# Performance work log

Hardware: AMD Instinct MI355X
Metric: run time of the kernel (lower is better)

The kernel has to match this reference:

```python
import jax, jax.numpy as jnp
import numpy as np

B, L, F, D = 128, 64, 3072, 1024
CV, CN = 512, 1024  # verb/noun concept channels
MAX_K = (L + 7) // 8
BN_EPS = 1e-5


def setup_inputs() -> dict:
    key = jax.random.key(0)
    ks = jax.random.split(key, 24)
    s_in = 1.0 / np.sqrt(F)
    s_d = 1.0 / np.sqrt(D)
    inp = {
        'inputs': jax.random.normal(ks[0], (B, L, F), jnp.float32),
        'input_lens': jax.random.randint(ks[1], (B,), 1, L + 1, jnp.int32),
        # three level linear embeds
        'W0': jax.random.normal(ks[2], (F, D), jnp.float32) * s_in,
        'b0': jnp.zeros((D,), jnp.float32),
        'W1': jax.random.normal(ks[3], (F, D), jnp.float32) * s_in,
        'b1': jnp.zeros((D,), jnp.float32),
        'W2': jax.random.normal(ks[4], (F, D), jnp.float32) * s_in,
        'b2': jnp.zeros((D,), jnp.float32),
        # attention scorer
        'w_attn': jax.random.normal(ks[5], (D, 1), jnp.float32) * s_d,
        'b_attn': jnp.zeros((1,), jnp.float32),
        # verb classifier: Conv1d(D, CV, 3, pad=1) + BN + sigmoid
        'Kv': jax.random.normal(ks[6], (CV, D, 3), jnp.float32) * (1.0 / np.sqrt(D * 3)),
        'bv': jnp.zeros((CV,), jnp.float32),
        'g_v': jnp.ones((CV,), jnp.float32),
        'beta_v': jnp.zeros((CV,), jnp.float32),
        'mean_v': jax.random.normal(ks[7], (CV,), jnp.float32) * 0.1,
        'var_v': jax.random.uniform(ks[8], (CV,), jnp.float32, 0.5, 1.5),
        # noun classifier: Conv1d(D, CN, 1) + BN + sigmoid
        'Kn': jax.random.normal(ks[9], (CN, D, 1), jnp.float32) * s_d,
        'bn_b': jnp.zeros((CN,), jnp.float32),
        'g_n': jnp.ones((CN,), jnp.float32),
        'beta_n': jnp.zeros((CN,), jnp.float32),
        'mean_n': jax.random.normal(ks[10], (CN,), jnp.float32) * 0.1,
        'var_n': jax.random.uniform(ks[11], (CN,), jnp.float32, 0.5, 1.5),
    }
    return inp


def _conv_bn_sigmoid(x_bld, K, b, gamma, beta, mean, var, pad):
    # x_bld: (B, L, D) -> permute to NCH (B, D, L) as in torch
    x = jnp.transpose(x_bld, (0, 2, 1))
    y = jax.lax.conv_general_dilated(
        x, K, window_strides=(1,), padding=[(pad, pad)],
        dimension_numbers=('NCH', 'OIH', 'NCH'))
    y = y + b[None, :, None]
    # BatchNorm1d in eval mode (running stats)
    y = (y - mean[None, :, None]) * jax.lax.rsqrt(var + BN_EPS)[None, :, None]
    y = y * gamma[None, :, None] + beta[None, :, None]
    y = jax.nn.sigmoid(y)
    return jnp.transpose(y, (0, 2, 1))  # (B, L, C)


def _topk_mean(logits, input_lens):
    # logits: (B, L, C); per-sample top-ceil(len/8) over time, then mean
    lens = input_lens.astype(jnp.int32)
    kk = (lens + 7) // 8  # (B,)
    valid = (jnp.arange(L)[None, :] < lens[:, None])  # (B, L)
    masked = jnp.where(valid[:, :, None], logits, -1e18)
    # top MAX_K per (batch, class) over time
    top = jax.lax.top_k(jnp.transpose(masked, (0, 2, 1)), MAX_K)[0]  # (B, C, MAX_K)
    take = (jnp.arange(MAX_K)[None, None, :] < kk[:, None, None]).astype(logits.dtype)
    return jnp.sum(top * take, axis=-1) / kk[:, None].astype(logits.dtype)  # (B, C)


def reference(inputs, input_lens, W0, b0, W1, b1, W2, b2, w_attn, b_attn,
              Kv, bv, g_v, beta_v, mean_v, var_v,
              Kn, bn_b, g_n, beta_n, mean_n, var_n):
    # level embeds (dropout is identity in eval)
    e0 = inputs @ W0 + b0
    e1 = inputs @ W1 + b1
    e2 = inputs @ W2 + b2

    # masked softmax attention pooling over time -> sent_embeds
    scores = (e0 @ w_attn)[:, :, 0] + b_attn[0]  # (B, L)
    valid = jnp.arange(L)[None, :] < input_lens[:, None]
    scores = jnp.where(valid, scores, -1e18)
    attn = jax.nn.softmax(scores, axis=1)
    sent_embeds = jnp.sum(e0 * attn[:, :, None], axis=1)  # (B, D)

    logits_verb = _conv_bn_sigmoid(e1, Kv, bv, g_v, beta_v, mean_v, var_v, pad=1)  # (B, L, CV)
    logits_noun = _conv_bn_sigmoid(e2, Kn, bn_b, g_n, beta_n, mean_n, var_n, pad=0)  # (B, L, CN)

    instance_logits_verb = _topk_mean(logits_verb, input_lens)  # (B, CV)
    instance_logits_noun = _topk_mean(logits_noun, input_lens)  # (B, CN)

    return (sent_embeds, e1, e2, instance_logits_verb, instance_logits_noun)
```

## Files before the change

### kernel.cpp

```cpp
#include <hip/hip_runtime.h>
#include <cstdint>
#include <cstddef>

typedef unsigned short u16;
typedef __attribute__((ext_vector_type(8))) short short8;
typedef __attribute__((ext_vector_type(4))) float f32x4;

static __device__ __forceinline__ float bf2f(u16 h) {
  union { unsigned u; float f; } a; a.u = ((unsigned)h) << 16; return a.f;
}
static __device__ __forceinline__ u16 f2bf(float x) {
  union { float f; unsigned u; } a; a.f = x;
  return (u16)((a.u + 0x7fffu + ((a.u >> 16) & 1u)) >> 16);
}

#define GLDS16(gp, lp)                                                          \
  __builtin_amdgcn_global_load_lds(                                             \
      (const __attribute__((address_space(1))) void*)(gp),                      \
      (__attribute__((address_space(3))) void*)(lp), 16, 0, 0)

__global__ void prep_all(const float* __restrict__ inputs, u16* __restrict__ Xbf,
                         const float* __restrict__ W0, const float* __restrict__ W1,
                         const float* __restrict__ W2, u16* __restrict__ Wt,
                         const float* __restrict__ Kv, const float* __restrict__ bv,
                         const float* __restrict__ g_v, const float* __restrict__ beta_v,
                         const float* __restrict__ mean_v, const float* __restrict__ var_v,
                         u16* __restrict__ KVt, float* __restrict__ biasv,
                         const float* __restrict__ Kn, const float* __restrict__ bnb,
                         const float* __restrict__ g_n, const float* __restrict__ beta_n,
                         const float* __restrict__ mean_n, const float* __restrict__ var_n,
                         u16* __restrict__ KNt, float* __restrict__ biasn,
                         u16* __restrict__ e1pad) {
  __shared__ float tile[32][33];
  const int id = blockIdx.x;
  const int tid = threadIdx.x;
  if (id < 24576) {
    const int i = id * 256 + tid;
    float4 v = ((const float4*)inputs)[i];
    ushort4 o;
    o.x = f2bf(v.x); o.y = f2bf(v.y); o.z = f2bf(v.z); o.w = f2bf(v.w);
    ((ushort4*)Xbf)[i] = o;
  } else if (id < 33792) {
    const int idd = id - 24576;
    const int kb = (idd % 96) * 32;
    const int jb = (idd / 96) * 32;
    const int tx = tid & 31, ty = tid >> 5;
    const int w = jb >> 10;
    const float* W = (w == 0) ? W0 : ((w == 1) ? W1 : W2);
    const int nb = jb & 1023;
    for (int i = ty; i < 32; i += 8)
      tile[i][tx] = W[(size_t)(kb + i) * 1024 + nb + tx];
    __syncthreads();
    for (int i = ty; i < 32; i += 8)
      Wt[(size_t)(jb + i) * 3072 + kb + tx] = f2bf(tile[tx][i]);
  } else if (id < 34304) {
    const int c = id - 33792;
    const float scale = g_v[c] * rsqrtf(var_v[c] + 1e-5f);
    for (int t = 0; t < 3; t++)
      for (int d = tid; d < 1024; d += 256)
        KVt[(size_t)c * 3072 + t * 1024 + d] = f2bf(Kv[(size_t)c * 3072 + d * 3 + t] * scale);
    if (tid == 0) biasv[c] = (bv[c] - mean_v[c]) * scale + beta_v[c];
  } else if (id < 35328) {
    const int c = id - 34304;
    const float scale = g_n[c] * rsqrtf(var_n[c] + 1e-5f);
    for (int d = tid; d < 1024; d += 256)
      KNt[(size_t)c * 1024 + d] = f2bf(Kn[(size_t)c * 1024 + d] * scale);
    if (tid == 0) biasn[c] = (bnb[c] - mean_n[c]) * scale + beta_n[c];
  } else {
    const int i = (id - 35328) * 256 + tid;
    const int b = i >> 11;
    const int j = i & 2047;
    const int r = (j < 1024) ? 0 : 65;
    const int d = j & 1023;
    e1pad[(size_t)(b * 66 + r) * 1024 + d] = 0;
  }
}

__global__ void gemm_embed(const u16* __restrict__ A, const u16* __restrict__ Bmat,
                           const float* __restrict__ bias0, const float* __restrict__ bias1,
                           const float* __restrict__ bias2,
                           float* __restrict__ oute1, float* __restrict__ oute2,
                           u16* __restrict__ e0bf, u16* __restrict__ e1pad,
                           u16* __restrict__ e2bf) {
  constexpr int K = 3072;
  __shared__ __align__(16) u16 As[128 * 32];
  __shared__ __align__(16) u16 Bs[128 * 32];

  const int tid = threadIdx.x;
  const int m0 = blockIdx.y * 128;
  const int n0 = blockIdx.x * 128;

  const int srow = tid >> 2;
  const int qlog = ((tid & 3) - (srow >> 1)) & 3;
  const int sq = qlog * 8;

  const u16* aR0 = A + (size_t)(m0 + srow) * 3072;
  const u16* aR1 = A + (size_t)(m0 + 64 + srow) * 3072;
  const u16* bR0 = Bmat + (size_t)(n0 + srow) * 3072;
  const u16* bR1 = Bmat + (size_t)(n0 + 64 + srow) * 3072;

  u16* ldsA0 = &As[tid * 8];
  u16* ldsA1 = &As[tid * 8 + 2048];
  u16* ldsB0 = &Bs[tid * 8];
  u16* ldsB1 = &Bs[tid * 8 + 2048];

  const int lane = tid & 63;
  const int warp = tid >> 6;
  const int wm = warp & 1, wn = warp >> 1;
  const int l15 = lane & 15, quad = lane >> 4;
  const int swz = (quad + (l15 >> 1)) & 3;

  const u16* aF = &As[(wm * 64 + l15) * 32 + swz * 8];
  const u16* bF = &Bs[(wn * 64 + l15) * 32 + swz * 8];

  f32x4 acc[4][4];
#pragma unroll
  for (int i = 0; i < 4; i++)
#pragma unroll
    for (int j = 0; j < 4; j++) acc[i][j] = (f32x4){0.f, 0.f, 0.f, 0.f};

  for (int k0 = 0; k0 < K; k0 += 32) {
    __syncthreads();
    GLDS16(aR0 + k0 + sq, ldsA0);
    GLDS16(aR1 + k0 + sq, ldsA1);
    GLDS16(bR0 + k0 + sq, ldsB0);
    GLDS16(bR1 + k0 + sq, ldsB1);
    __syncthreads();

    short8 fa[4], fb[4];
#pragma unroll
    for (int i = 0; i < 4; i++) fa[i] = *(const short8*)(aF + i * 512);
#pragma unroll
    for (int j = 0; j < 4; j++) fb[j] = *(const short8*)(bF + j * 512);
#pragma unroll
    for (int i = 0; i < 4; i++)
#pragma unroll
      for (int j = 0; j < 4; j++)
        acc[i][j] = __builtin_amdgcn_mfma_f32_16x16x32_bf16(fa[i], fb[j], acc[i][j], 0, 0, 0);
  }

  const int w = n0 >> 10;
  const float* bp = (w == 0) ? bias0 : ((w == 1) ? bias1 : bias2);
#pragma unroll
  for (int i = 0; i < 4; i++) {
    const int mrow = m0 + wm * 64 + i * 16 + quad * 4;
#pragma unroll
    for (int j = 0; j < 4; j++) {
      const int c = n0 + wn * 64 + j * 16 + l15;
      const int n = c & 1023;
      const float bias = bp[n];
#pragma unroll
      for (int r = 0; r < 4; r++) {
        const int m = mrow + r;
        const float v = acc[i][j][r] + bias;
        if (w == 0) {
          e0bf[(size_t)m * 1024 + n] = f2bf(v);
        } else if (w == 1) {
          oute1[(size_t)m * 1024 + n] = v;
          const int bb = m >> 6, ll = m & 63;
          e1pad[(size_t)(bb * 66 + ll + 1) * 1024 + n] = f2bf(v);
        } else {
          oute2[(size_t)m * 1024 + n] = v;
          e2bf[(size_t)m * 1024 + n] = f2bf(v);
        }
      }
    }
  }
}

template<int MODE>
__device__ __forceinline__ void conv_gemm_body(
    int bx, int by, const u16* __restrict__ A, const u16* __restrict__ Bmat,
    const float* __restrict__ bias, const int* __restrict__ lens,
    float* __restrict__ out, u16* As, u16* Bs) {
  constexpr int K = (MODE == 1) ? 3072 : 1024;
  constexpr int ldB = (MODE == 1) ? 3072 : 1024;
  constexpr int NC = (MODE == 1) ? 512 : 1024;

  const int tid = threadIdx.x;
  const int m0 = by * 128;
  const int n0 = bx * 128;

  const int srow = tid >> 2;
  const int qlog = ((tid & 3) - (srow >> 1)) & 3;
  const int sq = qlog * 8;

  const u16* aR0;
  const u16* aR1;
  int rb0 = 0, rb1 = 0;
  if constexpr (MODE == 1) {
    const int bb = m0 >> 6;
    rb0 = (bb * 66 + srow) * 1024;
    rb1 = ((bb + 1) * 66 + srow) * 1024;
    aR0 = A; aR1 = A;
  } else {
    aR0 = A + (size_t)(m0 + srow) * 1024;
    aR1 = A + (size_t)(m0 + 64 + srow) * 1024;
  }
  const u16* bR0 = Bmat + (size_t)(n0 + srow) * ldB;
  const u16* bR1 = Bmat + (size_t)(n0 + 64 + srow) * ldB;

  u16* ldsA0 = &As[tid * 8];
  u16* ldsA1 = &As[tid * 8 + 2048];
  u16* ldsB0 = &Bs[tid * 8];
  u16* ldsB1 = &Bs[tid * 8 + 2048];

  const int lane = tid & 63;
  const int warp = tid >> 6;
  const int wm = warp & 1, wn = warp >> 1;
  const int l15 = lane & 15, quad = lane >> 4;
  const int swz = (quad + (l15 >> 1)) & 3;

  const u16* aF = &As[(wm * 64 + l15) * 32 + swz * 8];
  const u16* bF = &Bs[(wn * 64 + l15) * 32 + swz * 8];

  f32x4 acc[4][4];
#pragma unroll
  for (int i = 0; i < 4; i++)
#pragma unroll
    for (int j = 0; j < 4; j++) acc[i][j] = (f32x4){0.f, 0.f, 0.f, 0.f};

  for (int k0 = 0; k0 < K; k0 += 32) {
    __syncthreads();
    const u16 *ga0, *ga1;
    if constexpr (MODE == 1) {
      const int t = k0 >> 10;
      const int kk = (k0 & 1023) + sq;
      ga0 = A + rb0 + t * 1024 + kk;
      ga1 = A + rb1 + t * 1024 + kk;
    } else {
      ga0 = aR0 + k0 + sq;
      ga1 = aR1 + k0 + sq;
    }
    GLDS16(ga0, ldsA0);
    GLDS16(ga1, ldsA1);
    GLDS16(bR0 + k0 + sq, ldsB0);
    GLDS16(bR1 + k0 + sq, ldsB1);
    __syncthreads();

    short8 fa[4], fb[4];
#pragma unroll
    for (int i = 0; i < 4; i++) fa[i] = *(const short8*)(aF + i * 512);
#pragma unroll
    for (int j = 0; j < 4; j++) fb[j] = *(const short8*)(bF + j * 512);
#pragma unroll
    for (int i = 0; i < 4; i++)
#pragma unroll
      for (int j = 0; j < 4; j++)
        acc[i][j] = __builtin_amdgcn_mfma_f32_16x16x32_bf16(fa[i], fb[j], acc[i][j], 0, 0, 0);
  }

  const int b = (m0 >> 6) + wm;
  const int len = lens[b];
  const int kk8 = (len + 7) >> 3;
#pragma unroll
  for (int j = 0; j < 4; j++) {
    const int c = n0 + wn * 64 + j * 16 + l15;
    const float bias_c = bias[c];
    float t[8];
#pragma unroll
    for (int q8 = 0; q8 < 8; q8++) t[q8] = -1e30f;
#pragma unroll
    for (int i = 0; i < 4; i++) {
#pragma unroll
      for (int r = 0; r < 4; r++) {
        const int l = i * 16 + quad * 4 + r;
        const float v = acc[i][j][r] + bias_c;
        const float sg = 1.0f / (1.0f + __expf(-v));
        float x = (l < len) ? sg : -1e30f;
#pragma unroll
        for (int q8 = 0; q8 < 8; q8++) {
          const float hi = fmaxf(t[q8], x);
          x = fminf(t[q8], x);
          t[q8] = hi;
        }
      }
    }
#pragma unroll
    for (int mask = 16; mask <= 32; mask <<= 1) {
      float xs[8];
#pragma unroll
      for (int q8 = 0; q8 < 8; q8++) xs[q8] = __shfl_xor(t[q8], mask);
#pragma unroll
      for (int q8 = 0; q8 < 8; q8++) {
        float x = xs[q8];
#pragma unroll
        for (int p8 = 0; p8 < 8; p8++) {
          const float hi = fmaxf(t[p8], x);
          x = fminf(t[p8], x);
          t[p8] = hi;
        }
      }
    }
    if (quad == 0) {
      float s = 0.f;
#pragma unroll
      for (int q8 = 0; q8 < 8; q8++) s += (q8 < kk8) ? t[q8] : 0.f;
      out[(size_t)b * NC + c] = s / (float)kk8;
    }
  }
}

__global__ void fused_tail(const u16* __restrict__ e1pad, const u16* __restrict__ KVt,
                           const float* __restrict__ biasv,
                           const u16* __restrict__ e2bf, const u16* __restrict__ KNt,
                           const float* __restrict__ biasn,
                           const u16* __restrict__ e0bf, const float* __restrict__ w_attn,
                           const float* __restrict__ b_attn, const int* __restrict__ lens,
                           float* __restrict__ out_sent, float* __restrict__ out_ilv,
                           float* __restrict__ out_iln) {
  __shared__ __align__(16) u16 smem[2 * 128 * 32 + 256];
  u16* As = smem;
  u16* Bs = smem + 128 * 32;
  const int id = blockIdx.x;
  if (id < 256) {
    conv_gemm_body<1>(id & 3, id >> 2, e1pad, KVt, biasv, lens, out_ilv, As, Bs);
  } else if (id < 768) {
    const int id2 = id - 256;
    conv_gemm_body<2>(id2 & 7, id2 >> 3, e2bf, KNt, biasn, lens, out_iln, As, Bs);
  } else {
    const int b = id - 768;
    const int tid = threadIdx.x;
    const int lane = tid & 63;
    const int warp = tid >> 6;
    float* sc = (float*)smem;
    float* at = sc + 64;
    const int len = lens[b];
    for (int t = 0; t < 16; t++) {
      const int l = warp * 16 + t;
      const u16* row = e0bf + (size_t)(b * 64 + l) * 1024;
      float s = 0.f;
#pragma unroll
      for (int u = 0; u < 16; u++) {
        const int d = lane + u * 64;
        s += bf2f(row[d]) * w_attn[d];
      }
#pragma unroll
      for (int off = 32; off > 0; off >>= 1) s += __shfl_down(s, off);
      if (lane == 0) sc[l] = s + b_attn[0];
    }
    __syncthreads();
    if (warp == 0) {
      float v = (lane < len) ? sc[lane] : -1e30f;
      float m = v;
#pragma unroll
      for (int off = 32; off > 0; off >>= 1) m = fmaxf(m, __shfl_xor(m, off));
      float p = (lane < len) ? __expf(v - m) : 0.f;
      float ssum = p;
#pragma unroll
      for (int off = 32; off > 0; off >>= 1) ssum += __shfl_xor(ssum, off);
      at[lane] = p / ssum;
    }
    __syncthreads();
    const int d0 = tid * 4;
    float a0 = 0.f, a1 = 0.f, a2 = 0.f, a3 = 0.f;
    for (int l = 0; l < 64; l++) {
      const float wgt = at[l];
      const ushort4 u4 = *(const ushort4*)(e0bf + (size_t)(b * 64 + l) * 1024 + d0);
      a0 += wgt * bf2f(u4.x);
      a1 += wgt * bf2f(u4.y);
      a2 += wgt * bf2f(u4.z);
      a3 += wgt * bf2f(u4.w);
    }
    float4 o; o.x = a0; o.y = a1; o.z = a2; o.w = a3;
    *(float4*)(out_sent + (size_t)b * 1024 + d0) = o;
  }
}

extern "C" void kernel_launch(void* const* d_in, const int* in_sizes, int n_in,
                              void* d_out, int out_size, void* d_ws, size_t ws_size,
                              hipStream_t stream) {
  const float* inputs = (const float*)d_in[0];
  const int*   lens   = (const int*)d_in[1];
  const float* W0 = (const float*)d_in[2];
  const float* b0 = (const float*)d_in[3];
  const float* W1 = (const float*)d_in[4];
  const float* b1 = (const float*)d_in[5];
  const float* W2 = (const float*)d_in[6];
  const float* b2 = (const float*)d_in[7];
  const float* w_attn = (const float*)d_in[8];
  const float* b_attn = (const float*)d_in[9];
  const float* Kv   = (const float*)d_in[10];
  const float* bv   = (const float*)d_in[11];
  const float* g_v  = (const float*)d_in[12];
  const float* beta_v = (const float*)d_in[13];
  const float* mean_v = (const float*)d_in[14];
  const float* var_v  = (const float*)d_in[15];
  const float* Kn   = (const float*)d_in[16];
  const float* bn_b = (const float*)d_in[17];
  const float* g_n  = (const float*)d_in[18];
  const float* beta_n = (const float*)d_in[19];
  const float* mean_n = (const float*)d_in[20];
  const float* var_n  = (const float*)d_in[21];

  float* out = (float*)d_out;
  float* out_sent = out;
  float* out_e1   = out + 131072;
  float* out_e2   = out + 131072 + 8388608;
  float* out_ilv  = out + 131072 + 2 * 8388608;
  float* out_iln  = out_ilv + 65536;

  char* p = (char*)d_ws;
  u16* Xbf  = (u16*)p; p += (size_t)8192 * 3072 * 2;
  u16* Wt   = (u16*)p; p += (size_t)3072 * 3072 * 2;
  u16* KVt  = (u16*)p; p += (size_t)512 * 3072 * 2;
  u16* KNt  = (u16*)p; p += (size_t)1024 * 1024 * 2;
  float* biasv = (float*)p; p += 512 * 4;
  float* biasn = (float*)p; p += 1024 * 4;
  u16* e0bf  = (u16*)p; p += (size_t)8192 * 1024 * 2;
  u16* e1pad = (u16*)p; p += (size_t)128 * 66 * 1024 * 2;
  u16* e2bf  = (u16*)p; p += (size_t)8192 * 1024 * 2;

  prep_all<<<36352, 256, 0, stream>>>(inputs, Xbf, W0, W1, W2, Wt,
                                      Kv, bv, g_v, beta_v, mean_v, var_v, KVt, biasv,
                                      Kn, bn_b, g_n, beta_n, mean_n, var_n, KNt, biasn,
                                      e1pad);
  gemm_embed<<<dim3(24, 64), 256, 0, stream>>>(Xbf, Wt, b0, b1, b2, out_e1, out_e2,
                                               e0bf, e1pad, e2bf);
  fused_tail<<<896, 256, 0, stream>>>(e1pad, KVt, biasv, e2bf, KNt, biasn,
                                      e0bf, w_attn, b_attn, lens,
                                      out_sent, out_ilv, out_iln);
}
```

Measured before the change: 518.5 us.

## Triple-buffer GEMM mainloop with async LDS loads and larger 128x256 tiles

Replaces the single-buffered, double-synchronized K loop with a shared three-slot software pipeline. Global-to-LDS loads for tile t+2 are issued while MFMAs run on tile t, using vmcnt waits, split barriers and s_setprio. K tiles grow to 64 and blocks to 512 threads covering 128x256 outputs. The same pipeline is used for the embedding GEMM and both conv/top-k GEMMs, so the tail grid shrinks. This aims to hide global memory latency and cut barrier overhead, at the cost of more LDS per block (144KB), lower occupancy and fragile hand-counted wait counts.

```diff
diff --git a/kernel.cpp b/kernel.cpp
--- a/kernel.cpp
+++ b/kernel.cpp
@@ -76,42 +76,195 @@
   }
 }
 
-__global__ void gemm_embed(const u16* __restrict__ A, const u16* __restrict__ Bmat,
-                           const float* __restrict__ bias0, const float* __restrict__ bias1,
-                           const float* __restrict__ bias2,
-                           float* __restrict__ oute1, float* __restrict__ oute2,
-                           u16* __restrict__ e0bf, u16* __restrict__ e1pad,
-                           u16* __restrict__ e2bf) {
-  constexpr int K = 3072;
-  __shared__ __align__(16) u16 As[128 * 32];
-  __shared__ __align__(16) u16 Bs[128 * 32];
-
+#define SLOT 24576
+
+#define MFMA16_()                                                                  \
+  acc[0][0] = __builtin_amdgcn_mfma_f32_16x16x32_bf16(a0, b0, acc[0][0], 0, 0, 0); \
+  acc[0][1] = __builtin_amdgcn_mfma_f32_16x16x32_bf16(a0, b1, acc[0][1], 0, 0, 0); \
+  acc[0][2] = __builtin_amdgcn_mfma_f32_16x16x32_bf16(a0, b2, acc[0][2], 0, 0, 0); \
+  acc[0][3] = __builtin_amdgcn_mfma_f32_16x16x32_bf16(a0, b3, acc[0][3], 0, 0, 0); \
+  acc[1][0] = __builtin_amdgcn_mfma_f32_16x16x32_bf16(a1, b0, acc[1][0], 0, 0, 0); \
+  acc[1][1] = __builtin_amdgcn_mfma_f32_16x16x32_bf16(a1, b1, acc[1][1], 0, 0, 0); \
+  acc[1][2] = __builtin_amdgcn_mfma_f32_16x16x32_bf16(a1, b2, acc[1][2], 0, 0, 0); \
+  acc[1][3] = __builtin_amdgcn_mfma_f32_16x16x32_bf16(a1, b3, acc[1][3], 0, 0, 0); \
+  acc[2][0] = __builtin_amdgcn_mfma_f32_16x16x32_bf16(a2, b0, acc[2][0], 0, 0, 0); \
+  acc[2][1] = __builtin_amdgcn_mfma_f32_16x16x32_bf16(a2, b1, acc[2][1], 0, 0, 0); \
+  acc[2][2] = __builtin_amdgcn_mfma_f32_16x16x32_bf16(a2, b2, acc[2][2], 0, 0, 0); \
+  acc[2][3] = __builtin_amdgcn_mfma_f32_16x16x32_bf16(a2, b3, acc[2][3], 0, 0, 0); \
+  acc[3][0] = __builtin_amdgcn_mfma_f32_16x16x32_bf16(a3, b0, acc[3][0], 0, 0, 0); \
+  acc[3][1] = __builtin_amdgcn_mfma_f32_16x16x32_bf16(a3, b1, acc[3][1], 0, 0, 0); \
+  acc[3][2] = __builtin_amdgcn_mfma_f32_16x16x32_bf16(a3, b2, acc[3][2], 0, 0, 0); \
+  acc[3][3] = __builtin_amdgcn_mfma_f32_16x16x32_bf16(a3, b3, acc[3][3], 0, 0, 0);
+
+#define KTILE_(CUR, NXT, T)                                                     \
+  {                                                                             \
+    const int t_ = (T);                                                         \
+    const bool st_ = (t_ + 2 < NT);                                             \
+    const size_t kk_ = (size_t)(t_ + 2) * 64;                                   \
+    {                                                      \
+      const u16* ra = rdA + (CUR) * SLOT;                                       \
+      const u16* rb = rdB + (CUR) * SLOT;                                       \
+      short8 a0 = *(const short8*)(ra + p0);                                    \
+      short8 a1 = *(const short8*)(ra + 1024 + p0);                             \
+      short8 a2 = *(const short8*)(ra + 2048 + p0);                             \
+      short8 a3 = *(const short8*)(ra + 3072 + p0);                             \
+      short8 b0 = *(const short8*)(rb + p0);                                    \
+      short8 b1 = *(const short8*)(rb + 1024 + p0);                             \
+      short8 b2 = *(const short8*)(rb + 2048 + p0);                             \
+      short8 b3 = *(const short8*)(rb + 3072 + p0);                             \
+      if (st_) {                                                                \
+        GLDS16(gA + kk_, stA + (NXT) * SLOT);                                   \
+        GLDS16(gA + hA + kk_, stA + (NXT) * SLOT + 4096);                       \
+        GLDS16(gB + kk_, stB + (NXT) * SLOT);                                   \
+      }                                                                         \
+      __builtin_amdgcn_s_barrier();                                             \
+      asm volatile("s_waitcnt lgkmcnt(0)" ::: "memory");                        \
+      __builtin_amdgcn_s_setprio(1);                                            \
+      MFMA16_();                                                                \
+      __builtin_amdgcn_s_setprio(0);                                            \
+      __builtin_amdgcn_s_barrier();                                             \
+    }                                                                           \
+    {                                                      \
+      const u16* ra = rdA + (CUR) * SLOT;                                       \
+      const u16* rb = rdB + (CUR) * SLOT;                                       \
+      short8 a0 = *(const short8*)(ra + p1);                                    \
+      short8 a1 = *(const short8*)(ra + 1024 + p1);                             \
+      short8 a2 = *(const short8*)(ra + 2048 + p1);                             \
+      short8 a3 = *(const short8*)(ra + 3072 + p1);                             \
+      short8 b0 = *(const short8*)(rb + p1);                                    \
+      short8 b1 = *(const short8*)(rb + 1024 + p1);                             \
+      short8 b2 = *(const short8*)(rb + 2048 + p1);                             \
+      short8 b3 = *(const short8*)(rb + 3072 + p1);                             \
+      if (st_) {                                                                \
+        GLDS16(gB + hB + kk_, stB + (NXT) * SLOT + 4096);                       \
+        GLDS16(gB + 2 * hB + kk_, stB + (NXT) * SLOT + 8192);                   \
+        GLDS16(gB + 3 * hB + kk_, stB + (NXT) * SLOT + 12288);                  \
+      }                                                                         \
+      __builtin_amdgcn_s_barrier();                                             \
+      asm volatile("s_waitcnt lgkmcnt(0)" ::: "memory");                        \
+      __builtin_amdgcn_s_setprio(1);                                            \
+      MFMA16_();                                                                \
+      __builtin_amdgcn_s_setprio(0);                                            \
+      if (t_ < NT - 2) {                                                        \
+        asm volatile("s_waitcnt vmcnt(6)" ::: "memory");                        \
+      } else if (t_ == NT - 2) {                                                \
+        asm volatile("s_waitcnt vmcnt(0)" ::: "memory");                        \
+      }                                                                         \
+      __builtin_amdgcn_s_barrier();                                             \
+    }                                                                           \
+  }
+
+template<int NT>
+static __device__ __forceinline__ void gemm_pipe(
+    const u16* __restrict__ gA, const size_t hA,
+    const u16* __restrict__ gB, const size_t hB,
+    u16* lds, f32x4 (&acc)[4][4]) {
   const int tid = threadIdx.x;
-  const int m0 = blockIdx.y * 128;
-  const int n0 = blockIdx.x * 128;
-
-  const int srow = tid >> 2;
-  const int qlog = ((tid & 3) - (srow >> 1)) & 3;
-  const int sq = qlog * 8;
-
-  const u16* aR0 = A + (size_t)(m0 + srow) * 3072;
-  const u16* aR1 = A + (size_t)(m0 + 64 + srow) * 3072;
-  const u16* bR0 = Bmat + (size_t)(n0 + srow) * 3072;
-  const u16* bR1 = Bmat + (size_t)(n0 + 64 + srow) * 3072;
-
-  u16* ldsA0 = &As[tid * 8];
-  u16* ldsA1 = &As[tid * 8 + 2048];
-  u16* ldsB0 = &Bs[tid * 8];
-  u16* ldsB1 = &Bs[tid * 8 + 2048];
-
   const int lane = tid & 63;
   const int warp = tid >> 6;
   const int wm = warp & 1, wn = warp >> 1;
   const int l15 = lane & 15, quad = lane >> 4;
-  const int swz = (quad + (l15 >> 1)) & 3;
-
-  const u16* aF = &As[(wm * 64 + l15) * 32 + swz * 8];
-  const u16* bF = &Bs[(wn * 64 + l15) * 32 + swz * 8];
+
+  u16* stA = lds + tid * 8;
+  u16* stB = lds + 8192 + tid * 8;
+  const u16* rdA = lds + (wm * 64 + l15) * 64;
+  const u16* rdB = lds + 8192 + (wn * 64 + l15) * 64;
+  const int p0 = ((quad + l15) & 7) * 8;
+  const int p1 = p0 ^ 32;
+
+#pragma unroll
+  for (int s = 0; s < 2; s++) {
+    const size_t kk = (size_t)s * 64;
+    GLDS16(gA + kk, stA + s * SLOT);
+    GLDS16(gA + hA + kk, stA + s * SLOT + 4096);
+    GLDS16(gB + kk, stB + s * SLOT);
+    GLDS16(gB + hB + kk, stB + s * SLOT + 4096);
+    GLDS16(gB + 2 * hB + kk, stB + s * SLOT + 8192);
+    GLDS16(gB + 3 * hB + kk, stB + s * SLOT + 12288);
+  }
+  asm volatile("s_waitcnt vmcnt(6)" ::: "memory");
+  __builtin_amdgcn_s_barrier();
+
+#pragma unroll 1
+  for (int t = 0; t < NT; t += 3) {
+    KTILE_(0, 2, t);
+    if (t + 1 < NT) KTILE_(1, 0, t + 1);
+    if (t + 2 < NT) KTILE_(2, 1, t + 2);
+  }
+}
+
+static __device__ __forceinline__ void topk_epilogue(
+    f32x4 (&acc)[4][4], const float* __restrict__ bias,
+    const int* __restrict__ lens, float* __restrict__ out,
+    const int NC, const int m0, const int n0) {
+  const int tid = threadIdx.x;
+  const int lane = tid & 63;
+  const int warp = tid >> 6;
+  const int wm = warp & 1, wn = warp >> 1;
+  const int l15 = lane & 15, quad = lane >> 4;
+  const int b = (m0 >> 6) + wm;
+  const int len = lens[b];
+  const int kk8 = (len + 7) >> 3;
+#pragma unroll
+  for (int j = 0; j < 4; j++) {
+    const int c = n0 + wn * 64 + j * 16 + l15;
+    const float bias_c = bias[c];
+    float t[8];
+#pragma unroll
+    for (int q8 = 0; q8 < 8; q8++) t[q8] = -1e30f;
+#pragma unroll
+    for (int i = 0; i < 4; i++) {
+#pragma unroll
+      for (int r = 0; r < 4; r++) {
+        const int l = i * 16 + quad * 4 + r;
+        const float v = acc[i][j][r] + bias_c;
+        const float sg = 1.0f / (1.0f + __expf(-v));
+        float x = (l < len) ? sg : -1e30f;
+#pragma unroll
+        for (int q8 = 0; q8 < 8; q8++) {
+          const float hi = fmaxf(t[q8], x);
+          x = fminf(t[q8], x);
+          t[q8] = hi;
+        }
+      }
+    }
+#pragma unroll
+    for (int mask = 16; mask <= 32; mask <<= 1) {
+      float xs[8];
+#pragma unroll
+      for (int q8 = 0; q8 < 8; q8++) xs[q8] = __shfl_xor(t[q8], mask);
+#pragma unroll
+      for (int q8 = 0; q8 < 8; q8++) {
+        float x = xs[q8];
+#pragma unroll
+        for (int p8 = 0; p8 < 8; p8++) {
+          const float hi = fmaxf(t[p8], x);
+          x = fminf(t[p8], x);
+          t[p8] = hi;
+        }
+      }
+    }
+    if (quad == 0) {
+      float s = 0.f;
+#pragma unroll
+      for (int q8 = 0; q8 < 8; q8++) s += (q8 < kk8) ? t[q8] : 0.f;
+      out[(size_t)b * NC + c] = s / (float)kk8;
+    }
+  }
+}
+
+__global__ __launch_bounds__(512, 2) void gemm_embed(
+    const u16* __restrict__ A, const u16* __restrict__ Bmat,
+    const float* __restrict__ bias0, const float* __restrict__ bias1,
+    const float* __restrict__ bias2,
+    float* __restrict__ oute1, float* __restrict__ oute2,
+    u16* __restrict__ e0bf, u16* __restrict__ e1pad, u16* __restrict__ e2bf) {
+  __shared__ __align__(16) u16 lds[3 * SLOT];
+  const int tid = threadIdx.x;
+  const int m0 = blockIdx.y * 128;
+  const int n0 = blockIdx.x * 256;
+  const int u = tid >> 3;
+  const int c8 = (((tid & 7) - u) & 7) * 8;
 
   f32x4 acc[4][4];
 #pragma unroll
@@ -119,26 +272,14 @@
 #pragma unroll
     for (int j = 0; j < 4; j++) acc[i][j] = (f32x4){0.f, 0.f, 0.f, 0.f};
 
-  for (int k0 = 0; k0 < K; k0 += 32) {
-    __syncthreads();
-    GLDS16(aR0 + k0 + sq, ldsA0);
-    GLDS16(aR1 + k0 + sq, ldsA1);
-    GLDS16(bR0 + k0 + sq, ldsB0);
-    GLDS16(bR1 + k0 + sq, ldsB1);
-    __syncthreads();
-
-    short8 fa[4], fb[4];
-#pragma unroll
-    for (int i = 0; i < 4; i++) fa[i] = *(const short8*)(aF + i * 512);
-#pragma unroll
-    for (int j = 0; j < 4; j++) fb[j] = *(const short8*)(bF + j * 512);
-#pragma unroll
-    for (int i = 0; i < 4; i++)
-#pragma unroll
-      for (int j = 0; j < 4; j++)
-        acc[i][j] = __builtin_amdgcn_mfma_f32_16x16x32_bf16(fa[i], fb[j], acc[i][j], 0, 0, 0);
-  }
-
+  gemm_pipe<48>(A + (size_t)(m0 + u) * 3072 + c8, (size_t)64 * 3072,
+                Bmat + (size_t)(n0 + u) * 3072 + c8, (size_t)64 * 3072,
+                lds, acc);
+
+  const int lane = tid & 63;
+  const int warp = tid >> 6;
+  const int wm = warp & 1, wn = warp >> 1;
+  const int l15 = lane & 15, quad = lane >> 4;
   const int w = n0 >> 10;
   const float* bp = (w == 0) ? bias0 : ((w == 1) ? bias1 : bias2);
 #pragma unroll
@@ -168,176 +309,63 @@
   }
 }
 
-template<int MODE>
-__device__ __forceinline__ void conv_gemm_body(
-    int bx, int by, const u16* __restrict__ A, const u16* __restrict__ Bmat,
-    const float* __restrict__ bias, const int* __restrict__ lens,
-    float* __restrict__ out, u16* As, u16* Bs) {
-  constexpr int K = (MODE == 1) ? 3072 : 1024;
-  constexpr int ldB = (MODE == 1) ? 3072 : 1024;
-  constexpr int NC = (MODE == 1) ? 512 : 1024;
-
+__global__ __launch_bounds__(512, 2) void fused_tail(
+    const u16* __restrict__ e1pad, const u16* __restrict__ KVt,
+    const float* __restrict__ biasv,
+    const u16* __restrict__ e2bf, const u16* __restrict__ KNt,
+    const float* __restrict__ biasn,
+    const u16* __restrict__ e0bf, const float* __restrict__ w_attn,
+    const float* __restrict__ b_attn, const int* __restrict__ lens,
+    float* __restrict__ out_sent, float* __restrict__ out_ilv,
+    float* __restrict__ out_iln) {
+  __shared__ __align__(16) u16 smem[3 * SLOT];
+  const int id = blockIdx.x;
   const int tid = threadIdx.x;
-  const int m0 = by * 128;
-  const int n0 = bx * 128;
-
-  const int srow = tid >> 2;
-  const int qlog = ((tid & 3) - (srow >> 1)) & 3;
-  const int sq = qlog * 8;
-
-  const u16* aR0;
-  const u16* aR1;
-  int rb0 = 0, rb1 = 0;
-  if constexpr (MODE == 1) {
-    const int bb = m0 >> 6;
-    rb0 = (bb * 66 + srow) * 1024;
-    rb1 = ((bb + 1) * 66 + srow) * 1024;
-    aR0 = A; aR1 = A;
+  if (id < 384) {
+    const int u = tid >> 3;
+    const int c8 = (((tid & 7) - u) & 7) * 8;
+    f32x4 acc[4][4];
+#pragma unroll
+    for (int i = 0; i < 4; i++)
+#pragma unroll
+      for (int j = 0; j < 4; j++) acc[i][j] = (f32x4){0.f, 0.f, 0.f, 0.f};
+    if (id < 128) {
+      const int by = id >> 1, bx = id & 1;
+      const int n0 = bx * 256;
+      gemm_pipe<48>(e1pad + ((size_t)(by * 2) * 66 + u) * 1024 + c8, (size_t)66 * 1024,
+                    KVt + (size_t)(n0 + u) * 3072 + c8, (size_t)64 * 3072,
+                    smem, acc);
+      topk_epilogue(acc, biasv, lens, out_ilv, 512, by * 128, n0);
+    } else {
+      const int id2 = id - 128;
+      const int by = id2 >> 2, bx = id2 & 3;
+      const int m0 = by * 128, n0 = bx * 256;
+      gemm_pipe<16>(e2bf + (size_t)(m0 + u) * 1024 + c8, (size_t)64 * 1024,
+                    KNt + (size_t)(n0 + u) * 1024 + c8, (size_t)64 * 1024,
+                    smem, acc);
+      topk_epilogue(acc, biasn, lens, out_iln, 1024, m0, n0);
+    }
   } else {
-    aR0 = A + (size_t)(m0 + srow) * 1024;
-    aR1 = A + (size_t)(m0 + 64 + srow) * 1024;
-  }
-  const u16* bR0 = Bmat + (size_t)(n0 + srow) * ldB;
-  const u16* bR1 = Bmat + (size_t)(n0 + 64 + srow) * ldB;
-
-  u16* ldsA0 = &As[tid * 8];
-  u16* ldsA1 = &As[tid * 8 + 2048];
-  u16* ldsB0 = &Bs[tid * 8];
-  u16* ldsB1 = &Bs[tid * 8 + 2048];
-
-  const int lane = tid & 63;
-  const int warp = tid >> 6;
-  const int wm = warp & 1, wn = warp >> 1;
-  const int l15 = lane & 15, quad = lane >> 4;
-  const int swz = (quad + (l15 >> 1)) & 3;
-
-  const u16* aF = &As[(wm * 64 + l15) * 32 + swz * 8];
-  const u16* bF = &Bs[(wn * 64 + l15) * 32 + swz * 8];
-
-  f32x4 acc[4][4];
-#pragma unroll
-  for (int i = 0; i < 4; i++)
-#pragma unroll
-    for (int j = 0; j < 4; j++) acc[i][j] = (f32x4){0.f, 0.f, 0.f, 0.f};
-
-  for (int k0 = 0; k0 < K; k0 += 32) {
-    __syncthreads();
-    const u16 *ga0, *ga1;
-    if constexpr (MODE == 1) {
-      const int t = k0 >> 10;
-      const int kk = (k0 & 1023) + sq;
-      ga0 = A + rb0 + t * 1024 + kk;
-      ga1 = A + rb1 + t * 1024 + kk;
-    } else {
-      ga0 = aR0 + k0 + sq;
-      ga1 = aR1 + k0 + sq;
-    }
-    GLDS16(ga0, ldsA0);
-    GLDS16(ga1, ldsA1);
-    GLDS16(bR0 + k0 + sq, ldsB0);
-    GLDS16(bR1 + k0 + sq, ldsB1);
-    __syncthreads();
-
-    short8 fa[4], fb[4];
-#pragma unroll
-    for (int i = 0; i < 4; i++) fa[i] = *(const short8*)(aF + i * 512);
-#pragma unroll
-    for (int j = 0; j < 4; j++) fb[j] = *(const short8*)(bF + j * 512);
-#pragma unroll
-    for (int i = 0; i < 4; i++)
-#pragma unroll
-      for (int j = 0; j < 4; j++)
-        acc[i][j] = __builtin_amdgcn_mfma_f32_16x16x32_bf16(fa[i], fb[j], acc[i][j], 0, 0, 0);
-  }
-
-  const int b = (m0 >> 6) + wm;
-  const int len = lens[b];
-  const int kk8 = (len + 7) >> 3;
-#pragma unroll
-  for (int j = 0; j < 4; j++) {
-    const int c = n0 + wn * 64 + j * 16 + l15;
-    const float bias_c = bias[c];
-    float t[8];
-#pragma unroll
-    for (int q8 = 0; q8 < 8; q8++) t[q8] = -1e30f;
-#pragma unroll
-    for (int i = 0; i < 4; i++) {
-#pragma unroll
-      for (int r = 0; r < 4; r++) {
-        const int l = i * 16 + quad * 4 + r;
-        const float v = acc[i][j][r] + bias_c;
-        const float sg = 1.0f / (1.0f + __expf(-v));
-        float x = (l < len) ? sg : -1e30f;
-#pragma unroll
-        for (int q8 = 0; q8 < 8; q8++) {
-          const float hi = fmaxf(t[q8], x);
-          x = fminf(t[q8], x);
-          t[q8] = hi;
-        }
-      }
-    }
-#pragma unroll
-    for (int mask = 16; mask <= 32; mask <<= 1) {
-      float xs[8];
-#pragma unroll
-      for (int q8 = 0; q8 < 8; q8++) xs[q8] = __shfl_xor(t[q8], mask);
-#pragma unroll
-      for (int q8 = 0; q8 < 8; q8++) {
-        float x = xs[q8];
-#pragma unroll
-        for (int p8 = 0; p8 < 8; p8++) {
-          const float hi = fmaxf(t[p8], x);
-          x = fminf(t[p8], x);
-          t[p8] = hi;
-        }
-      }
-    }
-    if (quad == 0) {
-      float s = 0.f;
-#pragma unroll
-      for (int q8 = 0; q8 < 8; q8++) s += (q8 < kk8) ? t[q8] : 0.f;
-      out[(size_t)b * NC + c] = s / (float)kk8;
-    }
-  }
-}
-
-__global__ void fused_tail(const u16* __restrict__ e1pad, const u16* __restrict__ KVt,
-                           const float* __restrict__ biasv,
-                           const u16* __restrict__ e2bf, const u16* __restrict__ KNt,
-                           const float* __restrict__ biasn,
-                           const u16* __restrict__ e0bf, const float* __restrict__ w_attn,
-                           const float* __restrict__ b_attn, const int* __restrict__ lens,
-                           float* __restrict__ out_sent, float* __restrict__ out_ilv,
-                           float* __restrict__ out_iln) {
-  __shared__ __align__(16) u16 smem[2 * 128 * 32 + 256];
-  u16* As = smem;
-  u16* Bs = smem + 128 * 32;
-  const int id = blockIdx.x;
-  if (id < 256) {
-    conv_gemm_body<1>(id & 3, id >> 2, e1pad, KVt, biasv, lens, out_ilv, As, Bs);
-  } else if (id < 768) {
-    const int id2 = id - 256;
-    conv_gemm_body<2>(id2 & 7, id2 >> 3, e2bf, KNt, biasn, lens, out_iln, As, Bs);
-  } else {
-    const int b = id - 768;
-    const int tid = threadIdx.x;
+    const int b = id - 384;
     const int lane = tid & 63;
     const int warp = tid >> 6;
     float* sc = (float*)smem;
     float* at = sc + 64;
     const int len = lens[b];
-    for (int t = 0; t < 16; t++) {
-      const int l = warp * 16 + t;
-      const u16* row = e0bf + (size_t)(b * 64 + l) * 1024;
-      float s = 0.f;
-#pragma unroll
-      for (int u = 0; u < 16; u++) {
-        const int d = lane + u * 64;
-        s += bf2f(row[d]) * w_attn[d];
+    if (warp < 4) {
+      for (int t = 0; t < 16; t++) {
+        const int l = warp * 16 + t;
+        const u16* row = e0bf + (size_t)(b * 64 + l) * 1024;
+        float s = 0.f;
+#pragma unroll
+        for (int uu = 0; uu < 16; uu++) {
+          const int d = lane + uu * 64;
+          s += bf2f(row[d]) * w_attn[d];
+        }
+#pragma unroll
+        for (int off = 32; off > 0; off >>= 1) s += __shfl_down(s, off);
+        if (lane == 0) sc[l] = s + b_attn[0];
       }
-#pragma unroll
-      for (int off = 32; off > 0; off >>= 1) s += __shfl_down(s, off);
-      if (lane == 0) sc[l] = s + b_attn[0];
     }
     __syncthreads();
     if (warp == 0) {
@@ -352,18 +380,20 @@
       at[lane] = p / ssum;
     }
     __syncthreads();
-    const int d0 = tid * 4;
-    float a0 = 0.f, a1 = 0.f, a2 = 0.f, a3 = 0.f;
-    for (int l = 0; l < 64; l++) {
-      const float wgt = at[l];
-      const ushort4 u4 = *(const ushort4*)(e0bf + (size_t)(b * 64 + l) * 1024 + d0);
-      a0 += wgt * bf2f(u4.x);
-      a1 += wgt * bf2f(u4.y);
-      a2 += wgt * bf2f(u4.z);
-      a3 += wgt * bf2f(u4.w);
-    }
-    float4 o; o.x = a0; o.y = a1; o.z = a2; o.w = a3;
-    *(float4*)(out_sent + (size_t)b * 1024 + d0) = o;
+    if (tid < 256) {
+      const int d0 = tid * 4;
+      float a0 = 0.f, a1 = 0.f, a2 = 0.f, a3 = 0.f;
+      for (int l = 0; l < 64; l++) {
+        const float wgt = at[l];
+        const ushort4 u4 = *(const ushort4*)(e0bf + (size_t)(b * 64 + l) * 1024 + d0);
+        a0 += wgt * bf2f(u4.x);
+        a1 += wgt * bf2f(u4.y);
+        a2 += wgt * bf2f(u4.z);
+        a3 += wgt * bf2f(u4.w);
+      }
+      float4 o; o.x = a0; o.y = a1; o.z = a2; o.w = a3;
+      *(float4*)(out_sent + (size_t)b * 1024 + d0) = o;
+    }
   }
 }
 
@@ -415,9 +445,9 @@
                                       Kv, bv, g_v, beta_v, mean_v, var_v, KVt, biasv,
                                       Kn, bn_b, g_n, beta_n, mean_n, var_n, KNt, biasn,
                                       e1pad);
-  gemm_embed<<<dim3(24, 64), 256, 0, stream>>>(Xbf, Wt, b0, b1, b2, out_e1, out_e2,
+  gemm_embed<<<dim3(12, 64), 512, 0, stream>>>(Xbf, Wt, b0, b1, b2, out_e1, out_e2,
                                                e0bf, e1pad, e2bf);
-  fused_tail<<<896, 256, 0, stream>>>(e1pad, KVt, biasv, e2bf, KNt, biasn,
+  fused_tail<<<512, 512, 0, stream>>>(e1pad, KVt, biasv, e2bf, KNt, biasn,
                                       e0bf, w_attn, b_attn, lens,
                                       out_sent, out_ilv, out_iln);
 }
```

Result: faster. 453.2 us (-12.6%).
